# Kernel tuning notes

Hardware: AMD Instinct MI355X
Metric: run time of the kernel (lower is better)

The kernel has to match this reference:

```python
import jax, jax.numpy as jnp
import numpy as np

D_MODEL = 1024
D_STATE = 16
EPS = 1e-5


def _layernorm(x, g, b):
    mu = x.mean(-1, keepdims=True)
    xc = x - mu
    var = (xc * xc).mean(-1, keepdims=True)
    return xc * jax.lax.rsqrt(var + EPS) * g + b


def setup_inputs() -> dict:
    key = jax.random.key(0)
    ks = jax.random.split(key, 10)
    B, L, d, n = 8, 1024, D_MODEL, D_STATE
    s = 1.0 / np.sqrt(d)
    return {
        "x": jax.random.normal(ks[0], (B, L, d), jnp.float32),
        "h_prev": jnp.zeros((B, d * n), jnp.float32),
        "ln_g": jnp.ones((d,), jnp.float32),
        "ln_b": jnp.zeros((d,), jnp.float32),
        "W_ig": jax.random.uniform(ks[1], (2 * d, d), jnp.float32, -s, s),
        "W_dt": jax.random.uniform(ks[2], (d, d), jnp.float32, -s, s),
        "b_dt": jax.random.uniform(ks[3], (d,), jnp.float32, -s, s),
        "A_log": jax.random.uniform(ks[4], (d, n), jnp.float32, -3.0, -1.0),
        "W_B": jax.random.uniform(ks[5], (n, d), jnp.float32, -s, s),
        "W_C": jax.random.uniform(ks[6], (n, d), jnp.float32, -s, s),
        "D": jnp.ones((d,), jnp.float32),
        "W_out": jax.random.uniform(ks[7], (d, d), jnp.float32, -s, s),
    }


def reference(x, h_prev, ln_g, ln_b, W_ig, W_dt, b_dt, A_log, W_B, W_C, D, W_out):
    Bsz, L, d = x.shape
    n = A_log.shape[1]
    x_norm = _layernorm(x, ln_g, ln_b)
    x_proj = jnp.einsum('bld,ed->ble', x_norm, W_ig)  # [B,L,2d]
    x_in, z = x_proj[..., :d], x_proj[..., d:]
    dt = jax.nn.softplus(jnp.einsum('bld,ed->ble', x_in, W_dt) + b_dt)  # [B,L,d]
    A = -jnp.exp(A_log)  # [d,n]
    B_t = jnp.einsum('bld,nd->bln', x_in, W_B)  # [B,L,n]
    C_t = jnp.einsum('bld,nd->bln', x_in, W_C)  # [B,L,n]
    h0 = h_prev.reshape(Bsz, d, n)

    def step(h, inp):
        dt_t, xin_t, Bt_t, Ct_t = inp  # [B,d],[B,d],[B,n],[B,n]
        dA = jnp.exp(dt_t[..., None] * A)                      # [B,d,n]
        h = dA * h + (dt_t * xin_t)[..., None] * Bt_t[:, None, :]
        y_t = (h * Ct_t[:, None, :]).sum(-1)                   # [B,d]
        return h, y_t

    xs = (jnp.swapaxes(dt, 0, 1), jnp.swapaxes(x_in, 0, 1),
          jnp.swapaxes(B_t, 0, 1), jnp.swapaxes(C_t, 0, 1))
    h_final, y = jax.lax.scan(step, h0, xs)
    y = jnp.swapaxes(y, 0, 1)  # [B,L,d]
    ssm_out = y * jax.nn.silu(z) + x_in * D
    out = jnp.einsum('bld,ed->ble', ssm_out, W_out)
    return (x + out, h_final.reshape(Bsz, -1))
```

## Files before the change

kernel.cpp:

```cpp
#include <hip/hip_runtime.h>
#include <hip/hip_bf16.h>
#include <math.h>

#define DM 1024
#define NS 16
#define BSZ 8
#define LSEQ 1024
#define MROWS (BSZ*LSEQ)
#define CH 32
#define ROWP 36

typedef __bf16 bf16;
typedef bf16 bf16x8 __attribute__((ext_vector_type(8)));
typedef bf16 bf16x4 __attribute__((ext_vector_type(4)));
typedef float f32x4 __attribute__((ext_vector_type(4)));
typedef unsigned int u32;
typedef unsigned short u16;
typedef u32 u32x4 __attribute__((ext_vector_type(4)));

__device__ __forceinline__ void async16(const void* g, void* l) {
  __builtin_amdgcn_global_load_lds((const __attribute__((address_space(1))) void*)g,
                                   (__attribute__((address_space(3))) void*)l,
                                   16, 0, 0);
}

__device__ __forceinline__ float bflo(u32 u) { return __builtin_bit_cast(float, (u32)(u << 16)); }
__device__ __forceinline__ float bfhi(u32 u) { return __builtin_bit_cast(float, (u32)(u & 0xffff0000u)); }

__global__ void cast_f2b(const float* __restrict__ s, bf16* __restrict__ d, int n4) {
  int i = blockIdx.x * 256 + threadIdx.x;
  if (i < n4) {
    float4 v = ((const float4*)s)[i];
    bf16x4 o;
    o.x = (bf16)v.x; o.y = (bf16)v.y; o.z = (bf16)v.z; o.w = (bf16)v.w;
    *(bf16x4*)(d + 4 * (size_t)i) = o;
  }
}

__global__ void transpose_cast(const float* __restrict__ src, bf16* __restrict__ dst) {
  __shared__ float tile[64][65];
  const int bk = blockIdx.x * 64;
  const int bd = blockIdx.y * 64;
  const int t = threadIdx.x;
  const int c4 = t & 15;
  const int r0 = t >> 4;
#pragma unroll
  for (int p = 0; p < 4; ++p) {
    int r = r0 + p * 16;
    float4 v = *(const float4*)(src + (size_t)(bd + r) * 1024 + bk + c4 * 4);
    tile[r][c4 * 4 + 0] = v.x;
    tile[r][c4 * 4 + 1] = v.y;
    tile[r][c4 * 4 + 2] = v.z;
    tile[r][c4 * 4 + 3] = v.w;
  }
  __syncthreads();
#pragma unroll
  for (int p = 0; p < 4; ++p) {
    int r = r0 + p * 16;
    bf16x4 o;
    o.x = (bf16)tile[c4 * 4 + 0][r];
    o.y = (bf16)tile[c4 * 4 + 1][r];
    o.z = (bf16)tile[c4 * 4 + 2][r];
    o.w = (bf16)tile[c4 * 4 + 3][r];
    *(bf16x4*)(dst + (size_t)(bk + r) * 1024 + bd + c4 * 4) = o;
  }
}

__global__ void ln_kernel(const float* __restrict__ x, const float* __restrict__ g,
                          const float* __restrict__ b, bf16* __restrict__ out) {
  const size_t row = blockIdx.x;
  const int t = threadIdx.x;
  float4 v = ((const float4*)(x + row * DM))[t];
  float s = v.x + v.y + v.z + v.w;
  float s2 = v.x*v.x + v.y*v.y + v.z*v.z + v.w*v.w;
#pragma unroll
  for (int m = 1; m < 64; m <<= 1) { s += __shfl_xor(s, m, 64); s2 += __shfl_xor(s2, m, 64); }
  __shared__ float red[8];
  int wave = t >> 6, lane = t & 63;
  if (lane == 0) { red[wave] = s; red[4 + wave] = s2; }
  __syncthreads();
  s  = red[0] + red[1] + red[2] + red[3];
  s2 = red[4] + red[5] + red[6] + red[7];
  float mu  = s * (1.f / DM);
  float var = s2 * (1.f / DM) - mu * mu;
  float inv = rsqrtf(var + 1e-5f);
  float4 gg = ((const float4*)g)[t];
  float4 bb = ((const float4*)b)[t];
  bf16x4 o;
  o.x = (bf16)((v.x - mu) * inv * gg.x + bb.x);
  o.y = (bf16)((v.y - mu) * inv * gg.y + bb.y);
  o.z = (bf16)((v.z - mu) * inv * gg.z + bb.z);
  o.w = (bf16)((v.w - mu) * inv * gg.w + bb.w);
  *(bf16x4*)(out + row * DM + t * 4) = o;
}

template <int EPI, bool SWZ>
__global__ __launch_bounds__(256)
void gemm_bf16(const bf16* __restrict__ A, const bf16* __restrict__ W, int K,
               float* __restrict__ out_f, bf16* __restrict__ out_b,
               u16* __restrict__ out_u1, u16* __restrict__ out_u2,
               const float* __restrict__ aux,
               float* __restrict__ out_f3, float* __restrict__ out_f4) {
  __shared__ bf16 As[2][128 * 32];
  __shared__ bf16 Bs[2][128 * 32];
  int tx, ty;
  if (SWZ) {
    int g = blockIdx.x;
    int xcd = g & 7, slot = g >> 3;
    tx = slot >> 3;
    ty = xcd * 8 + (slot & 7);
  } else {
    tx = blockIdx.x; ty = blockIdx.y;
  }
  const int tid  = threadIdx.x;
  const int wave = tid >> 6, lane = tid & 63;
  const int lr = lane & 15, quad = lane >> 4;
  const size_t arow = (size_t)ty * 128;
  const size_t brow = (size_t)tx * 128;
  f32x4 acc[4][4] = {};

  const int srl  = lane >> 2;
  const int kg   = lane & 3;
  const int srow = wave * 32 + srl;
  const int skc  = (kg ^ ((srl >> 1) & 3)) * 8;
  const bf16* ag = A + (arow + srow) * (size_t)K + skc;
  const bf16* wg = W + (brow + srow) * (size_t)K + skc;
  bf16* a_dst0 = &As[0][wave * 32 * 32];
  bf16* a_dst1 = &As[1][wave * 32 * 32];
  bf16* b_dst0 = &Bs[0][wave * 32 * 32];
  bf16* b_dst1 = &Bs[1][wave * 32 * 32];

  const int rk = (quad ^ ((lr >> 1) & 3)) * 8;
  const bf16* ap0 = &As[0][(((wave >> 1) * 64) + lr) * 32 + rk];
  const bf16* bp0 = &Bs[0][(((wave & 1) * 64) + lr) * 32 + rk];
  const bf16* ap1 = &As[1][(((wave >> 1) * 64) + lr) * 32 + rk];
  const bf16* bp1 = &Bs[1][(((wave & 1) * 64) + lr) * 32 + rk];

  auto STAGE = [&](bf16* adst, bf16* bdst, int kk) {
    async16(ag + kk,                       adst);
    async16(ag + (size_t)16 * K + kk,      adst + 16 * 32);
    async16(wg + kk,                       bdst);
    async16(wg + (size_t)16 * K + kk,      bdst + 16 * 32);
  };
  auto COMPUTE = [&](const bf16* ap, const bf16* bp) {
    bf16x8 af[4], bfr[4];
#pragma unroll
    for (int i = 0; i < 4; ++i) af[i] = *(const bf16x8*)(ap + i * 16 * 32);
#pragma unroll
    for (int j = 0; j < 4; ++j) bfr[j] = *(const bf16x8*)(bp + j * 16 * 32);
#pragma unroll
    for (int i = 0; i < 4; ++i)
#pragma unroll
      for (int j = 0; j < 4; ++j)
        acc[i][j] = __builtin_amdgcn_mfma_f32_16x16x32_bf16(af[i], bfr[j], acc[i][j], 0, 0, 0);
  };

  STAGE(a_dst0, b_dst0, 0);
  __syncthreads();
  for (int k0 = 0; k0 < K; k0 += 64) {
    STAGE(a_dst1, b_dst1, k0 + 32);
    COMPUTE(ap0, bp0);
    __syncthreads();
    if (k0 + 64 < K) STAGE(a_dst0, b_dst0, k0 + 64);
    COMPUTE(ap1, bp1);
    __syncthreads();
  }

  const size_t mbase = arow + (wave >> 1) * 64;
  const size_t nbase = brow + (wave & 1) * 64;
  if (EPI == 0) {
    if (nbase < DM) {
#pragma unroll
      for (int i = 0; i < 4; ++i)
#pragma unroll
        for (int j = 0; j < 4; ++j)
#pragma unroll
          for (int r = 0; r < 4; ++r) {
            size_t m = mbase + i * 16 + quad * 4 + r;
            size_t n = nbase + j * 16 + lr;
            out_u1[m * DM + n] = __builtin_bit_cast(u16, (bf16)acc[i][j][r]);
          }
    } else if (nbase < 2 * DM) {
#pragma unroll
      for (int i = 0; i < 4; ++i)
#pragma unroll
        for (int j = 0; j < 4; ++j)
#pragma unroll
          for (int r = 0; r < 4; ++r) {
            size_t m = mbase + i * 16 + quad * 4 + r;
            size_t n = nbase - DM + j * 16 + lr;
            out_b[m * DM + n] = (bf16)acc[i][j][r];
          }
    } else if (nbase < 3 * DM) {
#pragma unroll
      for (int i = 0; i < 4; ++i)
#pragma unroll
        for (int j = 0; j < 4; ++j)
#pragma unroll
          for (int r = 0; r < 4; ++r) {
            size_t m = mbase + i * 16 + quad * 4 + r;
            size_t n = nbase - 2 * DM + j * 16 + lr;
            float tt = acc[i][j][r] + aux[n];
            float sp = (tt > 20.f) ? tt : __logf(1.f + __expf(tt));
            out_u2[m * DM + n] = __builtin_bit_cast(u16, (bf16)sp);
          }
    } else if (nbase < 3 * DM + 2 * NS) {
#pragma unroll
      for (int i = 0; i < 4; ++i)
#pragma unroll
        for (int r = 0; r < 4; ++r) {
          size_t m = mbase + i * 16 + quad * 4 + r;
          out_f3[m * NS + lr] = acc[i][0][r];
          out_f4[m * NS + lr] = acc[i][1][r];
        }
    }
  } else {
#pragma unroll
    for (int i = 0; i < 4; ++i)
#pragma unroll
      for (int j = 0; j < 4; ++j)
#pragma unroll
        for (int r = 0; r < 4; ++r) {
          size_t m = mbase + i * 16 + quad * 4 + r;
          size_t n = nbase + j * 16 + lr;
          float v = acc[i][j][r];
          if (EPI == 2) {
            out_f[m * DM + n] = v + aux[m * DM + n];
          } else {
            out_b[m * (size_t)DM + n] = (bf16)v;
          }
        }
  }
}

__global__ __launch_bounds__(256)
void scan_kernel(const u16* __restrict__ dt_b, const u16* __restrict__ xi_b,
                 const bf16* __restrict__ z_b,
                 const float* __restrict__ B_t, const float* __restrict__ C_t,
                 const float* __restrict__ A_log, const float* __restrict__ h_prev,
                 const float* __restrict__ Dvec,
                 bf16* __restrict__ ssm_out, float* __restrict__ h_final) {
  const int blk = blockIdx.x;
  const int b = blk >> 6;
  const int d0 = (blk & 63) * 16;
  const int t = threadIdx.x;
  const int n = t & 15, dl = t >> 4;
  const int d = d0 + dl;
  const float Ac2 = -__expf(A_log[d * NS + n]) * 1.44269504f;
  float h = h_prev[(size_t)b * DM * NS + (size_t)d * NS + n];

  __shared__ u32   dxs[2][16][ROWP];
  __shared__ float Bsh[2][16][ROWP];
  __shared__ float Csh[2][16][ROWP];
  __shared__ float ys_p[CH][16][17];

  const size_t base_row = (size_t)b * LSEQ;
  const int l_a = t >> 4, c_a = t & 15;
  const float Dva = Dvec[d0 + c_a];

  {
    size_t ga = (base_row + l_a) * DM + d0 + c_a;
    size_t gb = (base_row + l_a + 16) * DM + d0 + c_a;
    dxs[0][c_a][l_a]      = (u32)dt_b[ga] | ((u32)xi_b[ga] << 16);
    dxs[0][c_a][l_a + 16] = (u32)dt_b[gb] | ((u32)xi_b[gb] << 16);
    size_t gB = base_row * NS;
    Bsh[0][c_a][l_a]      = B_t[gB + t];
    Csh[0][c_a][l_a]      = C_t[gB + t];
    Bsh[0][c_a][l_a + 16] = B_t[gB + t + 256];
    Csh[0][c_a][l_a + 16] = C_t[gB + t + 256];
  }
  float za = (float)z_b[(base_row + l_a) * DM + d0 + c_a];
  float zb = (float)z_b[(base_row + l_a + 16) * DM + d0 + c_a];
  __syncthreads();

  for (int c = 0; c < LSEQ / CH; ++c) {
    const int cur = c & 1, nxt = cur ^ 1;
    u32 pdxa, pdxb; float pBa, pBb, pCa, pCb, pza, pzb;
    if (c + 1 < LSEQ / CH) {
      size_t l0 = (size_t)(c + 1) * CH;
      size_t ga = (base_row + l0 + l_a) * DM + d0 + c_a;
      size_t gb = (base_row + l0 + l_a + 16) * DM + d0 + c_a;
      pdxa = (u32)dt_b[ga] | ((u32)xi_b[ga] << 16);
      pdxb = (u32)dt_b[gb] | ((u32)xi_b[gb] << 16);
      pza = (float)z_b[ga]; pzb = (float)z_b[gb];
      size_t gB = (base_row + l0) * NS;
      pBa = B_t[gB + t];       pCa = C_t[gB + t];
      pBb = B_t[gB + t + 256]; pCb = C_t[gB + t + 256];
    }
#pragma unroll
    for (int l4 = 0; l4 < CH; l4 += 4) {
      u32x4 dx4 = *(const u32x4*)&dxs[cur][dl][l4];
      f32x4 b4  = *(const f32x4*)&Bsh[cur][n][l4];
      f32x4 c4  = *(const f32x4*)&Csh[cur][n][l4];
#pragma unroll
      for (int i = 0; i < 4; ++i) {
        float dtv = bflo(dx4[i]), xiv = bfhi(dx4[i]);
        float a = __builtin_amdgcn_exp2f(dtv * Ac2);
        h = fmaf(a, h, (dtv * xiv) * b4[i]);
        ys_p[l4 + i][dl][n] = h * c4[i];
      }
    }
    __syncthreads();
    {
      float s1 = 0.f, s2 = 0.f;
#pragma unroll
      for (int k = 0; k < 16; ++k) {
        s1 += ys_p[l_a][c_a][k];
        s2 += ys_p[l_a + 16][c_a][k];
      }
      float x1 = bfhi(dxs[cur][c_a][l_a]);
      float x2 = bfhi(dxs[cur][c_a][l_a + 16]);
      float g1 = za / (1.f + __expf(-za));
      float g2 = zb / (1.f + __expf(-zb));
      size_t l0 = (size_t)c * CH;
      ssm_out[(base_row + l0 + l_a) * DM + d0 + c_a]      = (bf16)(s1 * g1 + x1 * Dva);
      ssm_out[(base_row + l0 + l_a + 16) * DM + d0 + c_a] = (bf16)(s2 * g2 + x2 * Dva);
    }
    if (c + 1 < LSEQ / CH) {
      dxs[nxt][c_a][l_a]      = pdxa;
      dxs[nxt][c_a][l_a + 16] = pdxb;
      Bsh[nxt][c_a][l_a]      = pBa;
      Csh[nxt][c_a][l_a]      = pCa;
      Bsh[nxt][c_a][l_a + 16] = pBb;
      Csh[nxt][c_a][l_a + 16] = pCb;
      za = pza; zb = pzb;
    }
    __syncthreads();
  }
  h_final[(size_t)b * DM * NS + (size_t)d0 * NS + t] = h;
}

extern "C" void kernel_launch(void* const* d_in, const int* in_sizes, int n_in,
                              void* d_out, int out_size, void* d_ws, size_t ws_size,
                              hipStream_t stream) {
  const float* x      = (const float*)d_in[0];
  const float* h_prev = (const float*)d_in[1];
  const float* ln_g   = (const float*)d_in[2];
  const float* ln_b   = (const float*)d_in[3];
  const float* W_ig   = (const float*)d_in[4];
  const float* W_dt   = (const float*)d_in[5];
  const float* b_dt   = (const float*)d_in[6];
  const float* A_log  = (const float*)d_in[7];
  const float* W_B    = (const float*)d_in[8];
  const float* W_C    = (const float*)d_in[9];
  const float* Dvec   = (const float*)d_in[10];
  const float* W_out  = (const float*)d_in[11];

  char* ws = (char*)d_ws;
  size_t off = 0;
  auto alloc = [&](size_t bytes) -> char* {
    char* p = ws + off;
    off += (bytes + 255) & ~(size_t)255;
    return p;
  };
  bf16*  wmega_b = (bf16*)alloc((size_t)3200 * DM * 2);
  bf16*  wstack_b= (bf16*)alloc((size_t)1152 * DM * 2);
  bf16*  wigT_b  = (bf16*)alloc((size_t)DM * DM * 2);
  bf16*  wout_b  = (bf16*)alloc((size_t)DM * DM * 2);
  bf16*  xnorm_b = (bf16*)alloc((size_t)MROWS * DM * 2);
  u16*   xi_w    = (u16*)alloc((size_t)MROWS * DM * 2);
  u16*   dt_w    = (u16*)alloc((size_t)MROWS * DM * 2);
  bf16*  z_bb    = (bf16*)alloc((size_t)MROWS * DM * 2);
  bf16*  ssm_b   = (bf16*)alloc((size_t)MROWS * DM * 2);
  float* Bt      = (float*)alloc((size_t)MROWS * NS * 4);
  float* Ct      = (float*)alloc((size_t)MROWS * NS * 4);
  (void)ws_size; (void)in_sizes; (void)n_in; (void)out_size;

  float* out_main = (float*)d_out;
  float* out_h    = (float*)d_out + (size_t)MROWS * DM;

  cast_f2b<<<(2 * DM * DM / 4 + 255) / 256, 256, 0, stream>>>(W_ig, wmega_b, 2 * DM * DM / 4);
  cast_f2b<<<(DM * DM / 4 + 255) / 256, 256, 0, stream>>>(W_dt, wstack_b, DM * DM / 4);
  cast_f2b<<<(NS * DM / 4 + 255) / 256, 256, 0, stream>>>(W_B, wstack_b + (size_t)DM * DM, NS * DM / 4);
  cast_f2b<<<(NS * DM / 4 + 255) / 256, 256, 0, stream>>>(W_C, wstack_b + (size_t)(DM + NS) * DM, NS * DM / 4);
  cast_f2b<<<(DM * DM / 4 + 255) / 256, 256, 0, stream>>>(W_out, wout_b, DM * DM / 4);
  transpose_cast<<<dim3(16, 16), 256, 0, stream>>>(W_ig, wigT_b);

  ln_kernel<<<MROWS, 256, 0, stream>>>(x, ln_g, ln_b, xnorm_b);

  gemm_bf16<3, false><<<dim3(8, 9), 256, 0, stream>>>(wstack_b, wigT_b, DM,
      nullptr, wmega_b + (size_t)2048 * DM, nullptr, nullptr, nullptr, nullptr, nullptr);

  gemm_bf16<0, true><<<1600, 256, 0, stream>>>(xnorm_b, wmega_b, DM,
      nullptr, z_bb, xi_w, dt_w, b_dt, Bt, Ct);

  scan_kernel<<<512, 256, 0, stream>>>(dt_w, xi_w, z_bb, Bt, Ct, A_log, h_prev,
                                       Dvec, ssm_b, out_h);

  gemm_bf16<2, true><<<512, 256, 0, stream>>>(ssm_b, wout_b, DM,
      out_main, nullptr, nullptr, nullptr, x, nullptr, nullptr);
}
```

Measured before the change: 358.3 us.

## Triple-buffer GEMM LDS staging with explicit vmcnt waits and one barrier per step

Changes the bf16 GEMM main loop from double buffering with two barriers per 64-wide k step to a three-stage ring of LDS buffers. Each 32-wide k step prefetches two tiles ahead and uses a partial s_waitcnt vmcnt(4) plus a raw s_barrier, so async global-to-LDS loads can overlap compute for longer. It costs 50% more LDS per block, which may lower occupancy, and it depends on the manual vmcnt counting being correct and the rotating pointers staying in registers.

Result: faster. 343.1 us (-4.2%).

```diff
diff --git a/kernel.cpp b/kernel.cpp
--- a/kernel.cpp
+++ b/kernel.cpp
@@ -101,8 +101,8 @@
                u16* __restrict__ out_u1, u16* __restrict__ out_u2,
                const float* __restrict__ aux,
                float* __restrict__ out_f3, float* __restrict__ out_f4) {
-  __shared__ bf16 As[2][128 * 32];
-  __shared__ bf16 Bs[2][128 * 32];
+  __shared__ bf16 As[3][128 * 32];
+  __shared__ bf16 Bs[3][128 * 32];
   int tx, ty;
   if (SWZ) {
     int g = blockIdx.x;
@@ -125,16 +125,15 @@
   const int skc  = (kg ^ ((srl >> 1) & 3)) * 8;
   const bf16* ag = A + (arow + srow) * (size_t)K + skc;
   const bf16* wg = W + (brow + srow) * (size_t)K + skc;
-  bf16* a_dst0 = &As[0][wave * 32 * 32];
-  bf16* a_dst1 = &As[1][wave * 32 * 32];
-  bf16* b_dst0 = &Bs[0][wave * 32 * 32];
-  bf16* b_dst1 = &Bs[1][wave * 32 * 32];
-
-  const int rk = (quad ^ ((lr >> 1) & 3)) * 8;
-  const bf16* ap0 = &As[0][(((wave >> 1) * 64) + lr) * 32 + rk];
-  const bf16* bp0 = &Bs[0][(((wave & 1) * 64) + lr) * 32 + rk];
-  const bf16* ap1 = &As[1][(((wave >> 1) * 64) + lr) * 32 + rk];
-  const bf16* bp1 = &Bs[1][(((wave & 1) * 64) + lr) * 32 + rk];
+
+  const int soff = wave * 32 * 32;
+  const int ra   = (((wave >> 1) * 64) + lr) * 32 + ((quad ^ ((lr >> 1) & 3)) * 8);
+  const int rb   = (((wave & 1)  * 64) + lr) * 32 + ((quad ^ ((lr >> 1) & 3)) * 8);
+
+  bf16 *aw0 = &As[0][soff], *aw1 = &As[1][soff], *aw2 = &As[2][soff];
+  bf16 *bw0 = &Bs[0][soff], *bw1 = &Bs[1][soff], *bw2 = &Bs[2][soff];
+  const bf16 *ar0 = &As[0][ra], *ar1 = &As[1][ra], *ar2 = &As[2][ra];
+  const bf16 *br0 = &Bs[0][rb], *br1 = &Bs[1][rb], *br2 = &Bs[2][rb];
 
   auto STAGE = [&](bf16* adst, bf16* bdst, int kk) {
     async16(ag + kk,                       adst);
@@ -155,15 +154,24 @@
         acc[i][j] = __builtin_amdgcn_mfma_f32_16x16x32_bf16(af[i], bfr[j], acc[i][j], 0, 0, 0);
   };
 
-  STAGE(a_dst0, b_dst0, 0);
-  __syncthreads();
-  for (int k0 = 0; k0 < K; k0 += 64) {
-    STAGE(a_dst1, b_dst1, k0 + 32);
-    COMPUTE(ap0, bp0);
-    __syncthreads();
-    if (k0 + 64 < K) STAGE(a_dst0, b_dst0, k0 + 64);
-    COMPUTE(ap1, bp1);
-    __syncthreads();
+  STAGE(aw0, bw0, 0);
+  STAGE(aw1, bw1, 32);
+  asm volatile("s_waitcnt vmcnt(4)" ::: "memory");
+  __builtin_amdgcn_s_barrier();
+
+  for (int k0 = 0; k0 < K; k0 += 32) {
+    const bool pf = (k0 + 64 < K);
+    if (pf) STAGE(aw2, bw2, k0 + 64);
+    COMPUTE(ar0, br0);
+    if (pf) asm volatile("s_waitcnt vmcnt(4)" ::: "memory");
+    else    asm volatile("s_waitcnt vmcnt(0)" ::: "memory");
+    __builtin_amdgcn_s_barrier();
+    bf16* t0;
+    t0 = aw0; aw0 = aw1; aw1 = aw2; aw2 = t0;
+    t0 = bw0; bw0 = bw1; bw1 = bw2; bw2 = t0;
+    const bf16* t1;
+    t1 = ar0; ar0 = ar1; ar1 = ar2; ar2 = t1;
+    t1 = br0; br0 = br1; br1 = br2; br2 = t1;
   }
 
   const size_t mbase = arow + (wave >> 1) * 64;
```
